# Optimization experiments

Measured on AMD Instinct MI355X. Metric: run time of the kernel, lower is better.

Reference implementation:

```python
import jax, jax.numpy as jnp
from jax import lax
import numpy as np

WINDOW_SIZE = 11
K1 = 0.01
K2 = 0.03
EPS = 1e-06


def _box_filter(x, k):
    """Depthwise uniform box filter with SAME (zero) padding, matching F.conv2d(..., groups=C)."""
    c = x.shape[1]
    kernel = jnp.full((c, 1, k, k), 1.0 / (k * k), dtype=x.dtype)  # [C,1,k,k]
    pad = k // 2
    return lax.conv_general_dilated(
        x, kernel,
        window_strides=(1, 1),
        padding=[(pad, pad), (pad, pad)],
        dimension_numbers=("NCHW", "OIHW", "NCHW"),
        feature_group_count=c,
    )


def setup_inputs() -> dict:
    key = jax.random.key(0)
    k1, k2 = jax.random.split(key)
    shape = (32, 3, 512, 512)
    pred = jax.random.uniform(k1, shape, dtype=jnp.float32)
    target = jax.random.uniform(k2, shape, dtype=jnp.float32)
    return {"pred": pred, "target": target}


def reference(pred, target):
    k = WINDOW_SIZE
    mu_p = _box_filter(pred, k)
    mu_t = _box_filter(target, k)
    sigma_p = _box_filter(pred * pred, k) - mu_p * mu_p
    sigma_t = _box_filter(target * target, k) - mu_t * mu_t
    sigma_x = _box_filter(pred * target, k) - mu_p * mu_t
    sigma_p = jnp.maximum(sigma_p, 0.0)
    sigma_t = jnp.maximum(sigma_t, 0.0)

    # per (batch, channel) dynamic range over spatial dims
    dyn_max = jnp.max(jnp.maximum(pred, target), axis=(-2, -1), keepdims=True)
    dyn_min = jnp.min(jnp.minimum(pred, target), axis=(-2, -1), keepdims=True)
    data_range = jnp.maximum(dyn_max - dyn_min, EPS)
    c1 = (K1 * data_range) ** 2
    c2 = (K2 * data_range) ** 2

    numerator = (2.0 * mu_p * mu_t + c1) * (2.0 * sigma_x + c2)
    denominator = (mu_p * mu_p + mu_t * mu_t + c1) * (sigma_p + sigma_t + c2)
    ssim_map = numerator / (denominator + EPS)
    loss_map = jnp.maximum((1.0 - ssim_map) * 0.5, 0.0)
    return jnp.mean(loss_map)
```

## Files before the change

kernel.cpp:

```cpp
#include <hip/hip_runtime.h>

constexpr int Wd = 512;
constexpr int PLANE = 512 * 512;

__global__ __launch_bounds__(256) void minmax_part(const float* __restrict__ pred,
                                                   const float* __restrict__ targ,
                                                   float* __restrict__ pmx,
                                                   float* __restrict__ pmn) {
    int bx = blockIdx.x;
    int plane = bx >> 3, seg = bx & 7;
    size_t base = (size_t)plane * PLANE + (size_t)seg * 32768;
    const float4* p4 = reinterpret_cast<const float4*>(pred + base);
    const float4* t4 = reinterpret_cast<const float4*>(targ + base);
    float mx = -3.0e38f, mn = 3.0e38f;
    for (int i = threadIdx.x; i < 8192; i += 256) {
        float4 a = p4[i], b = t4[i];
        mx = fmaxf(mx, fmaxf(fmaxf(fmaxf(a.x, b.x), fmaxf(a.y, b.y)),
                             fmaxf(fmaxf(a.z, b.z), fmaxf(a.w, b.w))));
        mn = fminf(mn, fminf(fminf(fminf(a.x, b.x), fminf(a.y, b.y)),
                             fminf(fminf(a.z, b.z), fminf(a.w, b.w))));
    }
    #pragma unroll
    for (int off = 32; off; off >>= 1) {
        mx = fmaxf(mx, __shfl_down(mx, off));
        mn = fminf(mn, __shfl_down(mn, off));
    }
    __shared__ float smx[4], smn[4];
    int wid = threadIdx.x >> 6, lane = threadIdx.x & 63;
    if (lane == 0) { smx[wid] = mx; smn[wid] = mn; }
    __syncthreads();
    if (threadIdx.x == 0) {
        pmx[bx] = fmaxf(fmaxf(smx[0], smx[1]), fmaxf(smx[2], smx[3]));
        pmn[bx] = fminf(fminf(smn[0], smn[1]), fminf(smn[2], smn[3]));
    }
}

__global__ void minmax_fin(const float* __restrict__ pmx, const float* __restrict__ pmn,
                           float* __restrict__ c1s, float* __restrict__ c2s, int planes) {
    int p = blockIdx.x * blockDim.x + threadIdx.x;
    if (p < planes) {
        float mx = -3.0e38f, mn = 3.0e38f;
        for (int s = 0; s < 8; ++s) {
            mx = fmaxf(mx, pmx[p * 8 + s]);
            mn = fminf(mn, pmn[p * 8 + s]);
        }
        float dr = fmaxf(mx - mn, 1e-6f);
        float a = 0.01f * dr, b = 0.03f * dr;
        c1s[p] = a * a;
        c2s[p] = b * b;
    }
}

__global__ __launch_bounds__(256) void ssim_main(const float* __restrict__ pred,
                                                 const float* __restrict__ targ,
                                                 const float* __restrict__ c1s,
                                                 const float* __restrict__ c2s,
                                                 float* __restrict__ parts) {
    __shared__ float red[4];
    int bx = blockIdx.x;
    int plane = bx >> 3, tile = bx & 7;
    int wid = threadIdx.x >> 6, c = threadIdx.x & 63;
    const float c1 = c1s[plane], c2 = c2s[plane];
    const float* Pg = pred + (size_t)plane * PLANE;
    const float* Tg = targ + (size_t)plane * PLANE;
    int r0 = tile * 64 + wid * 16;
    const bool lane0 = (c == 0), lane63 = (c == 63);

    float vsP[8], vsT[8], vsPP[8], vsTT[8], vsPT[8];
    #pragma unroll
    for (int k = 0; k < 8; ++k) { vsP[k] = 0; vsT[k] = 0; vsPP[k] = 0; vsTT[k] = 0; vsPT[k] = 0; }

    struct RowData { float4 a0, a1, b0, b1; };

    auto load_row = [&](int r) -> RowData {
        RowData d;
        if ((unsigned)r < 512u) {
            const float4* prow = reinterpret_cast<const float4*>(Pg + (size_t)r * Wd);
            const float4* trow = reinterpret_cast<const float4*>(Tg + (size_t)r * Wd);
            d.a0 = prow[2 * c]; d.a1 = prow[2 * c + 1];
            d.b0 = trow[2 * c]; d.b1 = trow[2 * c + 1];
        } else {
            d.a0 = d.a1 = d.b0 = d.b1 = make_float4(0, 0, 0, 0);
        }
        return d;
    };

    auto acc_data = [&](const RowData& d, bool add) {
        float pa[8] = {d.a0.x, d.a0.y, d.a0.z, d.a0.w, d.a1.x, d.a1.y, d.a1.z, d.a1.w};
        float tb[8] = {d.b0.x, d.b0.y, d.b0.z, d.b0.w, d.b1.x, d.b1.y, d.b1.z, d.b1.w};
        #pragma unroll
        for (int k = 0; k < 8; ++k) {
            if (add) {
                vsP[k]  += pa[k];
                vsT[k]  += tb[k];
                vsPP[k] = fmaf(pa[k], pa[k], vsPP[k]);
                vsTT[k] = fmaf(tb[k], tb[k], vsTT[k]);
                vsPT[k] = fmaf(pa[k], tb[k], vsPT[k]);
            } else {
                vsP[k]  -= pa[k];
                vsT[k]  -= tb[k];
                vsPP[k] = fmaf(-pa[k], pa[k], vsPP[k]);
                vsTT[k] = fmaf(-tb[k], tb[k], vsTT[k]);
                vsPT[k] = fmaf(-pa[k], tb[k], vsPT[k]);
            }
        }
    };

    auto hsum = [&](const float v[8], float H[8]) {
        float P[8];
        P[0] = v[0];
        #pragma unroll
        for (int k = 1; k < 8; ++k) P[k] = P[k - 1] + v[k];
        float T = P[7];
        float Tm  = __shfl_up(T, 1);
        float Pm2 = __shfl_up(P[2], 1);
        float Pm3 = __shfl_up(P[3], 1);
        float Pm4 = __shfl_up(P[4], 1);
        float Pm5 = __shfl_up(P[5], 1);
        float Pm6 = __shfl_up(P[6], 1);
        if (lane0) { Tm = 0; Pm2 = 0; Pm3 = 0; Pm4 = 0; Pm5 = 0; Pm6 = 0; }
        float Pp0 = __shfl_down(P[0], 1);
        float Pp1 = __shfl_down(P[1], 1);
        float Pp2 = __shfl_down(P[2], 1);
        float Pp3 = __shfl_down(P[3], 1);
        float Pp4 = __shfl_down(P[4], 1);
        if (lane63) { Pp0 = 0; Pp1 = 0; Pp2 = 0; Pp3 = 0; Pp4 = 0; }
        H[0] = (Tm - Pm2) + P[5];
        H[1] = (Tm - Pm3) + P[6];
        H[2] = (Tm - Pm4) + T;
        H[3] = (Tm - Pm5) + (T + Pp0);
        H[4] = (Tm - Pm6) + (T + Pp1);
        H[5] = T + Pp2;
        H[6] = (T - P[0]) + Pp3;
        H[7] = (T - P[1]) + Pp4;
    };

    float lsum = 0.0f;

    auto body = [&](int it, const RowData& E, const RowData& Lv, RowData& En, RowData& Ln) {
        En = load_row(r0 + it + 6);
        Ln = load_row(r0 + it - 4);

        acc_data(E, true);

        float H[5][8];
        hsum(vsP,  H[0]);
        hsum(vsT,  H[1]);
        hsum(vsPP, H[2]);
        hsum(vsTT, H[3]);
        hsum(vsPT, H[4]);

        constexpr float inv = 1.0f / 121.0f;
        #pragma unroll
        for (int i = 0; i < 8; ++i) {
            float mup = H[0][i] * inv, mut = H[1][i] * inv;
            float spp = fmaxf(H[2][i] * inv - mup * mup, 0.0f);
            float stt = fmaxf(H[3][i] * inv - mut * mut, 0.0f);
            float spt = H[4][i] * inv - mup * mut;
            float num = (2.0f * mup * mut + c1) * (2.0f * spt + c2);
            float den = (mup * mup + mut * mut + c1) * (spp + stt + c2);
            float ssim = __fdividef(num, den + 1e-6f);
            lsum += fmaxf((1.0f - ssim) * 0.5f, 0.0f);
        }
        acc_data(Lv, false);
    };

    for (int r = r0 - 5; r <= r0 + 4; ++r) acc_data(load_row(r), true);

    RowData E0 = load_row(r0 + 5);
    RowData L0 = load_row(r0 - 5);
    RowData E1, L1;

    #pragma unroll 1
    for (int it = 0; it < 16; it += 2) {
        body(it,     E0, L0, E1, L1);
        body(it + 1, E1, L1, E0, L0);
    }

    #pragma unroll
    for (int off = 32; off; off >>= 1) lsum += __shfl_down(lsum, off);
    if (c == 0) red[wid] = lsum;
    __syncthreads();
    if (threadIdx.x == 0) parts[bx] = (red[0] + red[1]) + (red[2] + red[3]);
}

__global__ void finish(const float* __restrict__ parts, float* __restrict__ out,
                       int n, float invN) {
    float s = 0.0f;
    for (int i = threadIdx.x; i < n; i += 256) s += parts[i];
    #pragma unroll
    for (int off = 32; off; off >>= 1) s += __shfl_down(s, off);
    __shared__ float sw[4];
    int wid = threadIdx.x >> 6, lane = threadIdx.x & 63;
    if (lane == 0) sw[wid] = s;
    __syncthreads();
    if (threadIdx.x == 0) out[0] = ((sw[0] + sw[1]) + (sw[2] + sw[3])) * invN;
}

extern "C" void kernel_launch(void* const* d_in, const int* in_sizes, int n_in,
                              void* d_out, int out_size, void* d_ws, size_t ws_size,
                              hipStream_t stream) {
    const float* pred = (const float*)d_in[0];
    const float* targ = (const float*)d_in[1];
    float* out = (float*)d_out;
    int planes = in_sizes[0] / PLANE;
    int G = planes * 8;

    float* ws   = (float*)d_ws;
    float* pmx  = ws;
    float* pmn  = ws + G;
    float* c1s  = ws + 2 * G;
    float* c2s  = ws + 2 * G + planes;
    float* prts = ws + 2 * G + 2 * planes;

    minmax_part<<<G, 256, 0, stream>>>(pred, targ, pmx, pmn);
    minmax_fin<<<(planes + 127) / 128, 128, 0, stream>>>(pmx, pmn, c1s, c2s, planes);
    ssim_main<<<G, 256, 0, stream>>>(pred, targ, c1s, c2s, prts);
    float invN = 1.0f / ((float)planes * (float)PLANE);
    finish<<<1, 256, 0, stream>>>(prts, out, G, invN);
}
```

Baseline: 125.1 us.

## Rescale SSIM math to raw window sums and give each wave 32 rows

Moves the SSIM formula into the unnormalised sum domain: the 1/121 scaling is folded into c1, c2 and the epsilon, which removes several multiplies per pixel. Each 64-lane wave now sweeps 32 rows instead of 16, so blocks shrink to 128 threads and the 10-row halo warm-up is amortised over twice as many output rows. The warm-up loads are also issued in batches of five rows to expose memory parallelism. Fewer waves per plane lowers overall parallelism, and the rescaled epsilon (121^4 * 1e-6) changes the rounding behaviour slightly.

```diff
diff --git a/kernel.cpp b/kernel.cpp
--- a/kernel.cpp
+++ b/kernel.cpp
@@ -45,25 +45,24 @@
             mn = fminf(mn, pmn[p * 8 + s]);
         }
         float dr = fmaxf(mx - mn, 1e-6f);
-        float a = 0.01f * dr, b = 0.03f * dr;
-        c1s[p] = a * a;
-        c2s[p] = b * b;
-    }
-}
-
-__global__ __launch_bounds__(256) void ssim_main(const float* __restrict__ pred,
+        c1s[p] = 1.4641f * dr * dr;
+        c2s[p] = 13.1769f * dr * dr;
+    }
+}
+
+__global__ __launch_bounds__(128) void ssim_main(const float* __restrict__ pred,
                                                  const float* __restrict__ targ,
                                                  const float* __restrict__ c1s,
                                                  const float* __restrict__ c2s,
                                                  float* __restrict__ parts) {
-    __shared__ float red[4];
+    __shared__ float red[2];
     int bx = blockIdx.x;
     int plane = bx >> 3, tile = bx & 7;
     int wid = threadIdx.x >> 6, c = threadIdx.x & 63;
     const float c1 = c1s[plane], c2 = c2s[plane];
     const float* Pg = pred + (size_t)plane * PLANE;
     const float* Tg = targ + (size_t)plane * PLANE;
-    int r0 = tile * 64 + wid * 16;
+    int r0 = tile * 64 + wid * 32;
     const bool lane0 = (c == 0), lane63 = (c == 63);
 
     float vsP[8], vsT[8], vsPP[8], vsTT[8], vsPT[8];
@@ -150,29 +149,38 @@
         hsum(vsTT, H[3]);
         hsum(vsPT, H[4]);
 
-        constexpr float inv = 1.0f / 121.0f;
         #pragma unroll
         for (int i = 0; i < 8; ++i) {
-            float mup = H[0][i] * inv, mut = H[1][i] * inv;
-            float spp = fmaxf(H[2][i] * inv - mup * mup, 0.0f);
-            float stt = fmaxf(H[3][i] * inv - mut * mut, 0.0f);
-            float spt = H[4][i] * inv - mup * mut;
-            float num = (2.0f * mup * mut + c1) * (2.0f * spt + c2);
-            float den = (mup * mup + mut * mut + c1) * (spp + stt + c2);
-            float ssim = __fdividef(num, den + 1e-6f);
+            float A = H[0][i], B = H[1][i];
+            float AB = A * B, A2 = A * A, B2 = B * B;
+            float t4 = fmaf(121.0f, H[4][i], -AB);
+            float num = (2.0f * AB + c1) * fmaf(2.0f, t4, c2);
+            float sp = fmaxf(fmaf(121.0f, H[2][i], -A2), 0.0f);
+            float st = fmaxf(fmaf(121.0f, H[3][i], -B2), 0.0f);
+            float den = (A2 + B2 + c1) * (sp + st + c2);
+            float ssim = __fdividef(num, den + 214.358881f);
             lsum += fmaxf((1.0f - ssim) * 0.5f, 0.0f);
         }
         acc_data(Lv, false);
     };
 
-    for (int r = r0 - 5; r <= r0 + 4; ++r) acc_data(load_row(r), true);
+    {
+        RowData D0 = load_row(r0 - 5), D1 = load_row(r0 - 4), D2 = load_row(r0 - 3),
+                D3 = load_row(r0 - 2), D4 = load_row(r0 - 1);
+        acc_data(D0, true); acc_data(D1, true); acc_data(D2, true);
+        acc_data(D3, true); acc_data(D4, true);
+        RowData D5 = load_row(r0 + 0), D6 = load_row(r0 + 1), D7 = load_row(r0 + 2),
+                D8 = load_row(r0 + 3), D9 = load_row(r0 + 4);
+        acc_data(D5, true); acc_data(D6, true); acc_data(D7, true);
+        acc_data(D8, true); acc_data(D9, true);
+    }
 
     RowData E0 = load_row(r0 + 5);
     RowData L0 = load_row(r0 - 5);
     RowData E1, L1;
 
     #pragma unroll 1
-    for (int it = 0; it < 16; it += 2) {
+    for (int it = 0; it < 32; it += 2) {
         body(it,     E0, L0, E1, L1);
         body(it + 1, E1, L1, E0, L0);
     }
@@ -181,7 +189,7 @@
     for (int off = 32; off; off >>= 1) lsum += __shfl_down(lsum, off);
     if (c == 0) red[wid] = lsum;
     __syncthreads();
-    if (threadIdx.x == 0) parts[bx] = (red[0] + red[1]) + (red[2] + red[3]);
+    if (threadIdx.x == 0) parts[bx] = red[0] + red[1];
 }
 
 __global__ void finish(const float* __restrict__ parts, float* __restrict__ out,
@@ -215,7 +223,7 @@
 
     minmax_part<<<G, 256, 0, stream>>>(pred, targ, pmx, pmn);
     minmax_fin<<<(planes + 127) / 128, 128, 0, stream>>>(pmx, pmn, c1s, c2s, planes);
-    ssim_main<<<G, 256, 0, stream>>>(pred, targ, c1s, c2s, prts);
+    ssim_main<<<G, 128, 0, stream>>>(pred, targ, c1s, c2s, prts);
     float invN = 1.0f / ((float)planes * (float)PLANE);
     finish<<<1, 256, 0, stream>>>(prts, out, G, invN);
 }
```

Measured after the change: 121.4 us. 3.0% less time.
